# Kernel tuning notes

Hardware: AMD Instinct MI355X
Metric: run time of the kernel (lower is better)

Reference implementation:

```python
import jax, jax.numpy as jnp
import numpy as np

N = 500000          # num vertices
E = 16000000        # num edges
VD = 3              # vertices_dim
EF = 2              # num_edge_features


def setup_inputs() -> dict:
    key = jax.random.key(0)
    ks = jax.random.split(key, 9)
    vertices = jax.random.normal(ks[0], (N, VD), dtype=jnp.float32)
    h_e2_prob = jax.random.uniform(ks[1], (E,), dtype=jnp.float32)
    edges = jax.random.randint(ks[2], (E, 2), 0, N, dtype=jnp.int64)
    # Linear params stored as [in, out] (transpose of torch's weight layout)
    We = jax.random.normal(ks[3], (2 * VD, EF), dtype=jnp.float32) * 0.1
    be = jax.random.normal(ks[4], (EF,), dtype=jnp.float32) * 0.1
    Wh = jax.random.normal(ks[5], (EF, VD), dtype=jnp.float32) * 0.1
    bh = jax.random.normal(ks[6], (VD,), dtype=jnp.float32) * 0.1
    Wv = jax.random.normal(ks[7], (VD, VD), dtype=jnp.float32) * 0.1
    bv = jax.random.normal(ks[8], (VD,), dtype=jnp.float32) * 0.1
    return {"vertices": vertices, "h_e2_prob": h_e2_prob, "edges": edges,
            "We": We, "be": be, "Wh": Wh, "bh": bh, "Wv": Wv, "bv": bv}


def reference(vertices, h_e2_prob, edges, We, be, Wh, bh, Wv, bv):
    # per-edge gather of endpoint features: [E, 2*VD]
    h_src = vertices[edges[:, 0]]
    h_tgt = vertices[edges[:, 1]]
    e_in = jnp.concatenate([h_src, h_tgt], axis=1)
    # h_ij = p_ij * f_e(cat(src, tgt))  -> [E, EF]
    h_ij = (e_in @ We + be) * h_e2_prob[:, None]
    # per-edge message f_h(h_ij) -> [E, VD]
    msg = h_ij @ Wh + bh
    # scatter-add messages into target nodes: h[j] += msg
    h = jax.ops.segment_sum(msg, edges[:, 1], num_segments=vertices.shape[0])
    # f_v(h) residual update
    return vertices + (h @ Wv + bv)
```

## Files before the change

### kernel.cpp

```cpp
#include <hip/hip_runtime.h>
#include <math.h>

#define NBMAX 512
#define GSCAT 512
#define BINW  1024
#define BSH   10
#define TBIG  1024
#define CH    4096

#define FIXSC  268435456.f
#define FIXINV (1.f/268435456.f)
#define BIASQ  (1ll<<30)

typedef int      vint4   __attribute__((ext_vector_type(4)));
typedef unsigned vuint4  __attribute__((ext_vector_type(4)));
typedef float    vfloat4 __attribute__((ext_vector_type(4)));


__global__ __launch_bounds__(256) void k_prep(
    const float* __restrict__ vertices, unsigned* __restrict__ aTp,
    const float* __restrict__ We, int n)
{
    int v = blockIdx.x * blockDim.x + threadIdx.x;
    if (v >= n) return;
    float v0 = vertices[3*v], v1 = vertices[3*v+1], v2 = vertices[3*v+2];
    float a0 = v0*We[0] + v1*We[2] + v2*We[4];
    float a1 = v0*We[1] + v1*We[3] + v2*We[5];
    unsigned u0 = __float_as_uint(a0);
    unsigned u1 = __float_as_uint(a1);
    u0 += 0x7FFFu + ((u0 >> 16) & 1u);
    u1 += 0x7FFFu + ((u1 >> 16) & 1u);
    aTp[v] = (u0 >> 16) | (u1 & 0xFFFF0000u);
}

__global__ __launch_bounds__(TBIG) void k_hist(
    const int* __restrict__ edges, unsigned* __restrict__ counts,
    int E, int per_block, int NB)
{
    __shared__ unsigned hist[NBMAX];
    int tid = threadIdx.x, b = blockIdx.x;
    for (int j = tid; j < NB; j += TBIG) hist[j] = 0;
    __syncthreads();
    int s0 = b * per_block;
    int s1 = min(E, s0 + per_block);
    int cnt = s1 - s0;
    if (cnt > 0) {
        int npair = cnt >> 1;
        for (int k = tid; k < npair; k += TBIG) {
            vint4 e2 = __builtin_nontemporal_load((const vint4*)&edges[2*(s0 + 2*k)]);
            atomicAdd(&hist[((unsigned)e2.y) >> BSH], 1u);
            atomicAdd(&hist[((unsigned)e2.w) >> BSH], 1u);
        }
        if ((cnt & 1) && tid == 0) {
            int t = ((const int2*)edges)[s1 - 1].y;
            atomicAdd(&hist[((unsigned)t) >> BSH], 1u);
        }
    }
    __syncthreads();
    for (int j = tid; j < NB; j += TBIG)
        counts[(size_t)b * NB + j] = hist[j];
}

__global__ __launch_bounds__(256) void k_scan(
    const unsigned* __restrict__ counts, unsigned* __restrict__ startm,
    unsigned* __restrict__ binFill, int NB, int cap)
{
    __shared__ unsigned c[GSCAT];
    __shared__ unsigned part[256];
    int j = blockIdx.x, tid = threadIdx.x;
    c[tid]       = counts[(size_t)tid * NB + j];
    c[tid + 256] = counts[(size_t)(tid + 256) * NB + j];
    __syncthreads();
    unsigned a0 = c[2*tid], a1 = c[2*tid+1];
    part[tid] = a0 + a1;
    __syncthreads();
    for (int off = 1; off < 256; off <<= 1) {
        unsigned u = (tid >= off) ? part[tid - off] : 0u;
        __syncthreads();
        part[tid] += u;
        __syncthreads();
    }
    unsigned incl = part[tid];
    unsigned base = (unsigned)j * (unsigned)cap;
    startm[(size_t)(2*tid)   * NB + j] = base + incl - a0 - a1;
    startm[(size_t)(2*tid+1) * NB + j] = base + incl - a1;
    if (tid == 255) binFill[j] = incl;
}

__global__ __launch_bounds__(TBIG) void k_scatter(
    const int* __restrict__ edges, const float* __restrict__ prob,
    const unsigned* __restrict__ startm, uint2* __restrict__ rec,
    int E, int per_block, int NB, int cap)
{
    __shared__ unsigned cur[NBMAX];
    __shared__ unsigned cnt[NBMAX];
    __shared__ unsigned sc[NBMAX];
    __shared__ unsigned wsum[8];
    __shared__ unsigned woff[8];
    __shared__ uint2    srec[CH];
    __shared__ unsigned short sbin[CH];

    int tid = threadIdx.x, b = blockIdx.x;
    for (int j = tid; j < NBMAX; j += TBIG) {
        cur[j] = (j < NB) ? startm[(size_t)b * NB + j] : 0u;
        cnt[j] = 0u;
    }
    __syncthreads();

    int s0 = b * per_block;
    int s1 = min(E, s0 + per_block);
    unsigned capu = (unsigned)cap;

    for (int cbase = s0; cbase < s1; cbase += CH) {
        int cc = min(CH, s1 - cbase);

        int idx = cbase + tid * 4;
        uint2    r[4];
        unsigned bn[4], rk[4];
        int nval = min(4, s1 - idx);
        if (nval == 4) {
            vint4   ea = __builtin_nontemporal_load((const vint4*)&edges[2*idx]);
            vint4   eb = __builtin_nontemporal_load((const vint4*)&edges[2*idx+4]);
            vfloat4 p4 = __builtin_nontemporal_load((const vfloat4*)&prob[idx]);
            int srcv[4] = { ea.x, ea.z, eb.x, eb.z };
            int tgtv[4] = { ea.y, ea.w, eb.y, eb.w };
            float pv[4] = { p4.x, p4.y, p4.z, p4.w };
            #pragma unroll
            for (int k = 0; k < 4; ++k) {
                unsigned t = (unsigned)tgtv[k];
                bn[k] = t >> BSH;
                r[k]  = make_uint2((unsigned)srcv[k] | ((t & (BINW-1u)) << 19),
                                   __float_as_uint(pv[k]));
                rk[k] = atomicAdd(&cnt[bn[k]], 1u);
            }
        } else if (nval > 0) {
            for (int k = 0; k < nval; ++k) {
                int2 st = ((const int2*)edges)[idx + k];
                float p = prob[idx + k];
                unsigned t = (unsigned)st.y;
                bn[k] = t >> BSH;
                r[k]  = make_uint2((unsigned)st.x | ((t & (BINW-1u)) << 19),
                                   __float_as_uint(p));
                rk[k] = atomicAdd(&cnt[bn[k]], 1u);
            }
        }
        __syncthreads();

        if (tid < NBMAX) {
            int lane = tid & 63, w = tid >> 6;
            unsigned incl = cnt[tid];
            #pragma unroll
            for (int off = 1; off < 64; off <<= 1) {
                unsigned u = __shfl_up(incl, off, 64);
                if (lane >= off) incl += u;
            }
            sc[tid] = incl;
            if (lane == 63) wsum[w] = incl;
        }
        __syncthreads();

        if (tid < 64) {
            unsigned v = (tid < 8) ? wsum[tid] : 0u;
            unsigned incl = v;
            #pragma unroll
            for (int off = 1; off < 8; off <<= 1) {
                unsigned u = __shfl_up(incl, off, 64);
                if (tid >= off) incl += u;
            }
            if (tid < 8) woff[tid] = incl - v;
        }
        __syncthreads();

        if (nval > 0) {
            for (int k = 0; k < nval; ++k) {
                unsigned bk = bn[k];
                unsigned ex = sc[bk] - cnt[bk] + woff[bk >> 6];
                unsigned sp = ex + rk[k];
                srec[sp] = r[k];
                sbin[sp] = (unsigned short)bk;
            }
        }
        __syncthreads();

        for (int i = tid; i < cc; i += TBIG) {
            unsigned bk = sbin[i];
            unsigned ex = sc[bk] - cnt[bk] + woff[bk >> 6];
            unsigned dst = cur[bk] + ((unsigned)i - ex);
            if (dst < (bk + 1u) * capu)
                rec[dst] = srec[i];
        }
        __syncthreads();

        for (int j = tid; j < NBMAX; j += TBIG) {
            if (j < NB) cur[j] += cnt[j];
            cnt[j] = 0u;
        }
        __syncthreads();
    }
}

__device__ __forceinline__ void accum_rec(
    unsigned rx, unsigned ry,
    const unsigned* __restrict__ aTp,
    const float* sB0, const float* sB1,
    unsigned long long* sG0, unsigned long long* sG1)
{
    if (rx & 0x80000000u) return;
    unsigned s  = rx & 0x7FFFFu;
    unsigned tl = rx >> 19;
    float p = __uint_as_float(ry);
    unsigned pk = aTp[s];
    float a0 = __uint_as_float(pk << 16);
    float a1 = __uint_as_float(pk & 0xFFFF0000u);
    float g0 = p * (a0 + sB0[tl]);
    float g1 = p * (a1 + sB1[tl]);
    g0 = fminf(fmaxf(g0, -3.9f), 3.9f);
    g1 = fminf(fmaxf(g1, -3.9f), 3.9f);
    unsigned long long q0 = (unsigned long long)(__float2ll_rn(g0 * FIXSC) + BIASQ) | (1ull << 48);
    unsigned long long q1 = (unsigned long long)(__float2ll_rn(g1 * FIXSC) + BIASQ);
    atomicAdd(&sG0[tl], q0);
    atomicAdd(&sG1[tl], q1);
}

__global__ __launch_bounds__(TBIG) void k_accum(
    const float* __restrict__ vertices,
    const unsigned* __restrict__ aTp,
    const uint2* __restrict__ rec, const unsigned* __restrict__ binFill,
    const float* __restrict__ We, const float* __restrict__ be,
    const float* __restrict__ Wh, const float* __restrict__ bh,
    const float* __restrict__ Wv, const float* __restrict__ bv,
    float* __restrict__ out, int n, int cap)
{
    __shared__ unsigned long long sG0[BINW], sG1[BINW];
    __shared__ float sB0[BINW], sB1[BINW];
    int j = blockIdx.x, tid = threadIdx.x;
    int v0 = j << BSH;
    int nv = min(BINW, n - v0);
    for (int k = tid; k < BINW; k += TBIG) {
        sG0[k] = 0ull; sG1[k] = 0ull;
        if (k < nv) {
            int v = v0 + k;
            float t0 = vertices[3*v], t1 = vertices[3*v+1], t2 = vertices[3*v+2];
            sB0[k] = t0*We[6] + t1*We[8] + t2*We[10] + be[0];
            sB1[k] = t0*We[7] + t1*We[9] + t2*We[11] + be[1];
        } else { sB0[k] = 0.f; sB1[k] = 0.f; }
    }
    __syncthreads();

    unsigned fill = binFill[j];
    const uint2* r2 = rec + (size_t)j * (size_t)cap;
    unsigned npair = fill >> 1;
    for (unsigned k = tid; k < npair; k += TBIG) {
        vuint4 rc = __builtin_nontemporal_load(&((const vuint4*)r2)[k]);
        accum_rec(rc.x, rc.y, aTp, sB0, sB1, sG0, sG1);
        accum_rec(rc.z, rc.w, aTp, sB0, sB1, sG0, sG1);
    }
    if ((fill & 1) && tid == 0) {
        uint2 rc = r2[fill - 1];
        accum_rec(rc.x, rc.y, aTp, sB0, sB1, sG0, sG1);
    }
    __syncthreads();

    if (tid < nv) {
        int v = v0 + tid;
        unsigned long long A = sG0[tid], B = sG1[tid];
        unsigned D = (unsigned)(A >> 48);
        long long is0 = (long long)(A & 0xFFFFFFFFFFFFull) - ((long long)D << 30);
        long long is1 = (long long)(B & 0xFFFFFFFFFFFFull) - ((long long)D << 30);
        float G0 = (float)is0 * FIXINV;
        float G1 = (float)is1 * FIXINV;
        float Df = (float)D;
        float h0 = G0*Wh[0] + G1*Wh[3] + Df*bh[0];
        float h1 = G0*Wh[1] + G1*Wh[4] + Df*bh[1];
        float h2 = G0*Wh[2] + G1*Wh[5] + Df*bh[2];
        float t0 = vertices[3*v], t1 = vertices[3*v+1], t2 = vertices[3*v+2];
        out[3*v+0] = t0 + bv[0] + h0*Wv[0] + h1*Wv[3] + h2*Wv[6];
        out[3*v+1] = t1 + bv[1] + h0*Wv[1] + h1*Wv[4] + h2*Wv[7];
        out[3*v+2] = t2 + bv[2] + h0*Wv[2] + h1*Wv[5] + h2*Wv[8];
    }
}


__device__ __forceinline__ void edge_math_full(
    const float* __restrict__ vertices, float p, int s, int t,
    const float* __restrict__ We, const float* __restrict__ be,
    const float* __restrict__ Wh, const float* __restrict__ bh,
    float& m0, float& m1, float& m2)
{
    float vs0 = vertices[3*s], vs1 = vertices[3*s+1], vs2 = vertices[3*s+2];
    float vt0 = vertices[3*t], vt1 = vertices[3*t+1], vt2 = vertices[3*t+2];
    float h0 = be[0] + vs0*We[0] + vs1*We[2] + vs2*We[4]
                     + vt0*We[6] + vt1*We[8] + vt2*We[10];
    float h1 = be[1] + vs0*We[1] + vs1*We[3] + vs2*We[5]
                     + vt0*We[7] + vt1*We[9] + vt2*We[11];
    h0 *= p; h1 *= p;
    m0 = bh[0] + h0*Wh[0] + h1*Wh[3];
    m1 = bh[1] + h0*Wh[1] + h1*Wh[4];
    m2 = bh[2] + h0*Wh[2] + h1*Wh[5];
}

__global__ __launch_bounds__(256) void gnn_edge_dev(
    const float* __restrict__ vertices, const float* __restrict__ prob,
    const int* __restrict__ edges,
    const float* __restrict__ We, const float* __restrict__ be,
    const float* __restrict__ Wh, const float* __restrict__ bh,
    float* __restrict__ acc, int E)
{
    int e = blockIdx.x * blockDim.x + threadIdx.x;
    if (e >= E) return;
    int2 st = ((const int2*)edges)[e];
    float m0, m1, m2;
    edge_math_full(vertices, prob[e], st.x, st.y, We, be, Wh, bh, m0, m1, m2);
    atomicAdd(&acc[3*st.y+0], m0);
    atomicAdd(&acc[3*st.y+1], m1);
    atomicAdd(&acc[3*st.y+2], m2);
}

__global__ __launch_bounds__(256) void gnn_vertex_inplace(
    const float* __restrict__ vertices,
    const float* __restrict__ Wv, const float* __restrict__ bv,
    float* __restrict__ out, int n)
{
    int v = blockIdx.x * blockDim.x + threadIdx.x;
    if (v >= n) return;
    float h0 = out[3*v+0], h1 = out[3*v+1], h2 = out[3*v+2];
    float o0 = vertices[3*v+0] + bv[0] + h0*Wv[0] + h1*Wv[3] + h2*Wv[6];
    float o1 = vertices[3*v+1] + bv[1] + h0*Wv[1] + h1*Wv[4] + h2*Wv[7];
    float o2 = vertices[3*v+2] + bv[2] + h0*Wv[2] + h1*Wv[5] + h2*Wv[8];
    out[3*v+0] = o0; out[3*v+1] = o1; out[3*v+2] = o2;
}


extern "C" void kernel_launch(void* const* d_in, const int* in_sizes, int n_in,
                              void* d_out, int out_size, void* d_ws, size_t ws_size,
                              hipStream_t stream)
{
    const float* vertices = (const float*)d_in[0];
    const float* prob     = (const float*)d_in[1];
    const int*   edges    = (const int*)d_in[2];
    const float* We       = (const float*)d_in[3];
    const float* be       = (const float*)d_in[4];
    const float* Wh       = (const float*)d_in[5];
    const float* bh       = (const float*)d_in[6];
    const float* Wv       = (const float*)d_in[7];
    const float* bv       = (const float*)d_in[8];
    float* out = (float*)d_out;

    const int E = in_sizes[2] / 2;
    const int n = in_sizes[0] / 3;

    const int NB = (n + BINW - 1) >> BSH;
    const int avg = E / NB;
    int cap = avg + 8 * (int)sqrt((double)avg);
    cap = (cap + 127) & ~127;

    size_t off = 0;
    unsigned* aTp     = (unsigned*)((char*)d_ws + off); off += (size_t)n * 4;
    off = (off + 255) & ~(size_t)255;
    unsigned* counts  = (unsigned*)((char*)d_ws + off); off += (size_t)GSCAT * NB * 4;
    unsigned* startm  = (unsigned*)((char*)d_ws + off); off += (size_t)GSCAT * NB * 4;
    unsigned* binFill = (unsigned*)((char*)d_ws + off); off += (size_t)NB * 4;
    off = (off + 255) & ~(size_t)255;
    uint2*    rec     = (uint2*)((char*)d_ws + off); off += (size_t)NB * cap * 8;
    const size_t need = off;

    if (NB <= NBMAX && n < (1 << 19) && ws_size >= need) {
        int per_block = (E + GSCAT - 1) / GSCAT;
        per_block = (per_block + 3) & ~3;
        k_prep<<<(n + 255)/256, 256, 0, stream>>>(vertices, aTp, We, n);
        k_hist<<<GSCAT, TBIG, 0, stream>>>(edges, counts, E, per_block, NB);
        k_scan<<<NB, 256, 0, stream>>>(counts, startm, binFill, NB, cap);
        k_scatter<<<GSCAT, TBIG, 0, stream>>>(edges, prob, startm, rec,
                                              E, per_block, NB, cap);
        k_accum<<<NB, TBIG, 0, stream>>>(vertices, aTp, rec, binFill,
                                         We, be, Wh, bh, Wv, bv, out, n, cap);
    } else {
        hipMemsetAsync(d_out, 0, (size_t)out_size * sizeof(float), stream);
        gnn_edge_dev<<<(E + 255)/256, 256, 0, stream>>>(vertices, prob, edges,
                                                        We, be, Wh, bh, out, E);
        gnn_vertex_inplace<<<(n + 255)/256, 256, 0, stream>>>(vertices, Wv, bv, out, n);
    }
}
```

Measured before the change: 227.2 us.

## Pack bin id into record, quantize prob, double scatter chunk

```diff
diff --git a/kernel.cpp b/kernel.cpp
--- a/kernel.cpp
+++ b/kernel.cpp
@@ -6,11 +6,13 @@
 #define BINW  1024
 #define BSH   10
 #define TBIG  1024
-#define CH    4096
+#define CH    8192
 
 #define FIXSC  268435456.f
 #define FIXINV (1.f/268435456.f)
 #define BIASQ  (1ll<<30)
+#define PQS    4194304.f
+#define PQINV  (1.f/4194304.f)
 
 typedef int      vint4   __attribute__((ext_vector_type(4)));
 typedef unsigned vuint4  __attribute__((ext_vector_type(4)));
@@ -95,10 +97,11 @@
     __shared__ unsigned cur[NBMAX];
     __shared__ unsigned cnt[NBMAX];
     __shared__ unsigned sc[NBMAX];
+    __shared__ unsigned exl[NBMAX];
+    __shared__ unsigned exo[NBMAX];
     __shared__ unsigned wsum[8];
     __shared__ unsigned woff[8];
     __shared__ uint2    srec[CH];
-    __shared__ unsigned short sbin[CH];
 
     int tid = threadIdx.x, b = blockIdx.x;
     for (int j = tid; j < NBMAX; j += TBIG) {
@@ -114,23 +117,27 @@
     for (int cbase = s0; cbase < s1; cbase += CH) {
         int cc = min(CH, s1 - cbase);
 
-        int idx = cbase + tid * 4;
-        uint2    r[4];
-        unsigned bn[4], rk[4];
-        int nval = min(4, s1 - idx);
-        if (nval == 4) {
+        int idx = cbase + tid * 8;
+        uint2    r[8];
+        unsigned bn[8], rk[8];
+        int nval = min(8, s1 - idx);
+        if (nval == 8) {
             vint4   ea = __builtin_nontemporal_load((const vint4*)&edges[2*idx]);
             vint4   eb = __builtin_nontemporal_load((const vint4*)&edges[2*idx+4]);
-            vfloat4 p4 = __builtin_nontemporal_load((const vfloat4*)&prob[idx]);
-            int srcv[4] = { ea.x, ea.z, eb.x, eb.z };
-            int tgtv[4] = { ea.y, ea.w, eb.y, eb.w };
-            float pv[4] = { p4.x, p4.y, p4.z, p4.w };
+            vint4   ec = __builtin_nontemporal_load((const vint4*)&edges[2*idx+8]);
+            vint4   ed = __builtin_nontemporal_load((const vint4*)&edges[2*idx+12]);
+            vfloat4 pa = __builtin_nontemporal_load((const vfloat4*)&prob[idx]);
+            vfloat4 pb = __builtin_nontemporal_load((const vfloat4*)&prob[idx+4]);
+            int srcv[8] = { ea.x, ea.z, eb.x, eb.z, ec.x, ec.z, ed.x, ed.z };
+            int tgtv[8] = { ea.y, ea.w, eb.y, eb.w, ec.y, ec.w, ed.y, ed.w };
+            float pv[8] = { pa.x, pa.y, pa.z, pa.w, pb.x, pb.y, pb.z, pb.w };
             #pragma unroll
-            for (int k = 0; k < 4; ++k) {
+            for (int k = 0; k < 8; ++k) {
                 unsigned t = (unsigned)tgtv[k];
                 bn[k] = t >> BSH;
+                unsigned pq = min(__float2uint_rn(pv[k] * PQS), 0x3FFFFFu);
                 r[k]  = make_uint2((unsigned)srcv[k] | ((t & (BINW-1u)) << 19),
-                                   __float_as_uint(pv[k]));
+                                   (bn[k] << 22) | pq);
                 rk[k] = atomicAdd(&cnt[bn[k]], 1u);
             }
         } else if (nval > 0) {
@@ -139,8 +146,9 @@
                 float p = prob[idx + k];
                 unsigned t = (unsigned)st.y;
                 bn[k] = t >> BSH;
+                unsigned pq = min(__float2uint_rn(p * PQS), 0x3FFFFFu);
                 r[k]  = make_uint2((unsigned)st.x | ((t & (BINW-1u)) << 19),
-                                   __float_as_uint(p));
+                                   (bn[k] << 22) | pq);
                 rk[k] = atomicAdd(&cnt[bn[k]], 1u);
             }
         }
@@ -171,23 +179,25 @@
         }
         __syncthreads();
 
+        if (tid < NBMAX) {
+            unsigned ex = sc[tid] - cnt[tid] + woff[tid >> 6];
+            exl[tid] = ex;
+            exo[tid] = cur[tid] - ex;
+        }
+        __syncthreads();
+
         if (nval > 0) {
-            for (int k = 0; k < nval; ++k) {
-                unsigned bk = bn[k];
-                unsigned ex = sc[bk] - cnt[bk] + woff[bk >> 6];
-                unsigned sp = ex + rk[k];
-                srec[sp] = r[k];
-                sbin[sp] = (unsigned short)bk;
-            }
+            for (int k = 0; k < nval; ++k)
+                srec[exl[bn[k]] + rk[k]] = r[k];
         }
         __syncthreads();
 
         for (int i = tid; i < cc; i += TBIG) {
-            unsigned bk = sbin[i];
-            unsigned ex = sc[bk] - cnt[bk] + woff[bk >> 6];
-            unsigned dst = cur[bk] + ((unsigned)i - ex);
+            uint2 rr = srec[i];
+            unsigned bk = rr.y >> 22;
+            unsigned dst = exo[bk] + (unsigned)i;
             if (dst < (bk + 1u) * capu)
-                rec[dst] = srec[i];
+                rec[dst] = rr;
         }
         __syncthreads();
 
@@ -205,10 +215,9 @@
     const float* sB0, const float* sB1,
     unsigned long long* sG0, unsigned long long* sG1)
 {
-    if (rx & 0x80000000u) return;
     unsigned s  = rx & 0x7FFFFu;
-    unsigned tl = rx >> 19;
-    float p = __uint_as_float(ry);
+    unsigned tl = (rx >> 19) & 0x3FFu;
+    float p = (float)(ry & 0x3FFFFFu) * PQINV;
     unsigned pk = aTp[s];
     float a0 = __uint_as_float(pk << 16);
     float a1 = __uint_as_float(pk & 0xFFFF0000u);
@@ -366,7 +375,7 @@
 
     if (NB <= NBMAX && n < (1 << 19) && ws_size >= need) {
         int per_block = (E + GSCAT - 1) / GSCAT;
-        per_block = (per_block + 3) & ~3;
+        per_block = (per_block + 7) & ~7;
         k_prep<<<(n + 255)/256, 256, 0, stream>>>(vertices, aTp, We, n);
         k_hist<<<GSCAT, TBIG, 0, stream>>>(edges, counts, E, per_block, NB);
         k_scan<<<NB, 256, 0, stream>>>(counts, startm, binFill, NB, cap);
```

Measured after the change: 248.0 us. 9.2% more time.
